# Performance work log

Measured on AMD Instinct MI355X. Metric: run time of the kernel, lower is better.

The kernel has to match this reference:

```python
import jax, jax.numpy as jnp
import numpy as np

D = 256      # dim
H = 8        # num_heads
HD = D // H  # head dim
P = 256      # patch_size
B = 4        # num clouds
L = 32768    # points per cloud (divisible by P)
N = B * L
MLP = int(D * 2.0)
PEH = max(32, D // 4)
EPS = 1e-5


def setup_inputs() -> dict:
    key = jax.random.key(0)
    ks = jax.random.split(key, 20)
    s = 0.02
    w = lambda k, shp: jax.random.normal(k, shp, jnp.float32) * s
    inp = {
        "feats": jax.random.normal(ks[0], (N, D), jnp.float32),
        "coord": jax.random.uniform(ks[1], (N, 3), jnp.float32),
        "lengths": jnp.full((B,), L, jnp.int32),
        # CoordPositionalEncoding: Linear(3,PEH) -> ReLU -> Linear(PEH,D)
        "pe_w1": w(ks[2], (3, PEH)), "pe_b1": jnp.zeros((PEH,), jnp.float32),
        "pe_w2": w(ks[3], (PEH, D)), "pe_b2": jnp.zeros((D,), jnp.float32),
        "pre_g": jnp.ones((D,), jnp.float32), "pre_b": jnp.zeros((D,), jnp.float32),
        # block: norm1 + MHA + norm2 + MLP
        "n1_g": jnp.ones((D,), jnp.float32), "n1_b": jnp.zeros((D,), jnp.float32),
        "wqkv": w(ks[4], (D, 3 * D)), "bqkv": jnp.zeros((3 * D,), jnp.float32),
        "wo": w(ks[5], (D, D)), "bo": jnp.zeros((D,), jnp.float32),
        "n2_g": jnp.ones((D,), jnp.float32), "n2_b": jnp.zeros((D,), jnp.float32),
        "m_w1": w(ks[6], (D, MLP)), "m_b1": jnp.zeros((MLP,), jnp.float32),
        "m_w2": w(ks[7], (MLP, D)), "m_b2": jnp.zeros((D,), jnp.float32),
        # global_gate: Linear(2D,D)->ReLU->Linear(D,D)->Sigmoid
        "gg_w1": w(ks[8], (2 * D, D)), "gg_b1": jnp.zeros((D,), jnp.float32),
        "gg_w2": w(ks[9], (D, D)), "gg_b2": jnp.zeros((D,), jnp.float32),
        # fuse: Linear(2D,D)->ReLU->Linear(D,D)
        "f_w1": w(ks[10], (2 * D, D)), "f_b1": jnp.zeros((D,), jnp.float32),
        "f_w2": w(ks[11], (D, D)), "f_b2": jnp.zeros((D,), jnp.float32),
    }
    return inp


def _ln(x, g, b):
    m = x.mean(-1, keepdims=True)
    v = jnp.mean((x - m) ** 2, -1, keepdims=True)
    return (x - m) * jax.lax.rsqrt(v + EPS) * g + b


def _sgca(feats, coord, lengths,
          pe_w1, pe_b1, pe_w2, pe_b2, pre_g, pre_b,
          n1_g, n1_b, wqkv, bqkv, wo, bo, n2_g, n2_b,
          m_w1, m_b1, m_w2, m_b2,
          gg_w1, gg_b1, gg_w2, gg_b2, f_w1, f_b1, f_w2, f_b2):
    Bn = lengths.shape[0]
    Ln = feats.shape[0] // Bn  # equal-length clouds

    def cloud(f, c):  # f: [L, D], c: [L, 3]
        # positional encoding (per-cloud centered / max-abs scaled coords)
        cc = c - c.mean(0, keepdims=True)
        scale = jnp.clip(jnp.abs(cc).max(0, keepdims=True), 1e-6)
        pe = jax.nn.relu((cc / scale) @ pe_w1 + pe_b1) @ pe_w2 + pe_b2
        x = _ln(f + pe, pre_g, pre_b)
        # serialization order from min-max normalized coords
        cn = c - c.min(0, keepdims=True)
        cn = cn / jnp.clip(cn.max(0, keepdims=True), 1e-6)
        key = cn[:, 0] + 2.17 * cn[:, 1] + 3.31 * cn[:, 2]
        order = jnp.argsort(key)
        xs = x[order].reshape(-1, P, D)  # [NP, P, D] block-diagonal windows
        # attention block (pre-norm MHA + residual)
        h = _ln(xs, n1_g, n1_b)
        qkv = h @ wqkv + bqkv
        q = qkv[..., :D].reshape(-1, P, H, HD)
        k = qkv[..., D:2 * D].reshape(-1, P, H, HD)
        v = qkv[..., 2 * D:].reshape(-1, P, H, HD)
        scores = jnp.einsum('nphd,nqhd->nhpq', q, k) / np.sqrt(HD).astype(np.float32)
        a = jax.nn.softmax(scores, axis=-1)
        o = jnp.einsum('nhpq,nqhd->nphd', a, v).reshape(-1, P, D)
        xs = xs + (o @ wo + bo)
        # MLP + residual
        xs = xs + (jax.nn.gelu(_ln(xs, n2_g, n2_b) @ m_w1 + m_b1, approximate=False) @ m_w2 + m_b2)
        # undo serialization
        xo = xs.reshape(-1, D)[jnp.argsort(order)]
        # global token gate/fuse
        gt = jnp.broadcast_to(xo.mean(0, keepdims=True), xo.shape)
        gate = jax.nn.sigmoid(jax.nn.relu(jnp.concatenate([f, gt], -1) @ gg_w1 + gg_b1) @ gg_w2 + gg_b2)
        fused = jax.nn.relu(jnp.concatenate([xo, gt], -1) @ f_w1 + f_b1) @ f_w2 + f_b2
        return f + gate * fused

    out = jax.vmap(cloud)(feats.reshape(Bn, Ln, D), coord.reshape(Bn, Ln, 3))
    return out.reshape(-1, D)


def reference(feats, coord, lengths,
              pe_w1, pe_b1, pe_w2, pe_b2, pre_g, pre_b,
              n1_g, n1_b, wqkv, bqkv, wo, bo, n2_g, n2_b,
              m_w1, m_b1, m_w2, m_b2,
              gg_w1, gg_b1, gg_w2, gg_b2, f_w1, f_b1, f_w2, f_b2):
    return _sgca(feats, coord, lengths,
                 pe_w1, pe_b1, pe_w2, pe_b2, pre_g, pre_b,
                 n1_g, n1_b, wqkv, bqkv, wo, bo, n2_g, n2_b,
                 m_w1, m_b1, m_w2, m_b2,
                 gg_w1, gg_b1, gg_w2, gg_b2, f_w1, f_b1, f_w2, f_b2)
```

## Files before the change

kernel.cpp:

```cpp
#include <hip/hip_runtime.h>
#include <hip/hip_bf16.h>
#include <math.h>

#define D_DIM 256
#define NHEAD 8
#define HDIM 32
#define PATCH 256
#define NCLOUD 4
#define LPC 32768
#define NTOT (NCLOUD * LPC)
#define MLPD 512
#define PEHID 64
#define LN_EPS 1e-5f
#define NCHUNK 4
#define CROWS (NTOT / NCHUNK)

typedef unsigned long long u64;
typedef unsigned short u16;
typedef short bf16x8 __attribute__((ext_vector_type(8)));
typedef float f32x4 __attribute__((ext_vector_type(4)));

__device__ __forceinline__ u16 f2bf(float x) {
  unsigned u = __float_as_uint(x);
  u += 0x7fffu + ((u >> 16) & 1u);
  return (u16)(u >> 16);
}
__device__ __forceinline__ float bf2f(u16 u) {
  return __uint_as_float(((unsigned)u) << 16);
}

__device__ __forceinline__ void gload_lds16(const u16* g, u16* l) {
  __builtin_amdgcn_global_load_lds((const __attribute__((address_space(1))) void*)g,
                                   (__attribute__((address_space(3))) void*)l, 16, 0, 0);
}

__global__ __launch_bounds__(256) void stats_kernel(const float* __restrict__ coord,
                                                    float* __restrict__ stats) {
  const int c = blockIdx.x, t = threadIdx.x;
  float sm[3] = {0.f, 0.f, 0.f};
  float mn[3] = {1e30f, 1e30f, 1e30f};
  float mx[3] = {-1e30f, -1e30f, -1e30f};
  const float* cp = coord + (size_t)c * LPC * 3;
  for (int i = t; i < LPC; i += 256) {
#pragma unroll
    for (int a = 0; a < 3; a++) {
      float v = cp[(size_t)i * 3 + a];
      sm[a] += v;
      mn[a] = fminf(mn[a], v);
      mx[a] = fmaxf(mx[a], v);
    }
  }
  __shared__ float sb[256];
  float rsum[3], rmn[3], rmx[3];
#pragma unroll
  for (int a = 0; a < 3; a++) {
    sb[t] = sm[a]; __syncthreads();
    for (int s = 128; s > 0; s >>= 1) { if (t < s) sb[t] += sb[t + s]; __syncthreads(); }
    rsum[a] = sb[0]; __syncthreads();
    sb[t] = mn[a]; __syncthreads();
    for (int s = 128; s > 0; s >>= 1) { if (t < s) sb[t] = fminf(sb[t], sb[t + s]); __syncthreads(); }
    rmn[a] = sb[0]; __syncthreads();
    sb[t] = mx[a]; __syncthreads();
    for (int s = 128; s > 0; s >>= 1) { if (t < s) sb[t] = fmaxf(sb[t], sb[t + s]); __syncthreads(); }
    rmx[a] = sb[0]; __syncthreads();
  }
  if (t == 0) {
    float* st = stats + c * 16;
#pragma unroll
    for (int a = 0; a < 3; a++) {
      float mean = rsum[a] / (float)LPC;
      st[a] = mean;
      st[3 + a] = fmaxf(fmaxf(rmx[a] - mean, mean - rmn[a]), 1e-6f);
      st[6 + a] = rmn[a];
      st[9 + a] = fmaxf(rmx[a] - rmn[a], 1e-6f);
    }
  }
}

__global__ __launch_bounds__(256) void key_kernel(const float* __restrict__ coord,
                                                  const float* __restrict__ stats,
                                                  u64* __restrict__ keys) {
#pragma clang fp contract(off)
  const int g = blockIdx.x * 256 + threadIdx.x;
  const int c = g >> 15;
  const float* st = stats + c * 16;
  float k0 = (coord[(size_t)g * 3 + 0] - st[6]) / st[9];
  float k1 = (coord[(size_t)g * 3 + 1] - st[7]) / st[10];
  float k2 = (coord[(size_t)g * 3 + 2] - st[8]) / st[11];
  float key = k0 + 2.17f * k1;
  key = key + 3.31f * k2;
  keys[g] = ((u64)__float_as_uint(key) << 32) | (unsigned)(g & (LPC - 1));
}

__global__ __launch_bounds__(1024) void sort_local_kernel(u64* __restrict__ keys) {
  __shared__ u64 s[4096];
  const int base = blockIdx.x * 4096;
  const int t = threadIdx.x;
  for (int i = t; i < 4096; i += 1024) s[i] = keys[base + i];
  __syncthreads();
  for (int k = 2; k <= 4096; k <<= 1) {
    for (int j = k >> 1; j > 0; j >>= 1) {
      for (int p = t; p < 2048; p += 1024) {
        int i = ((p & ~(j - 1)) << 1) | (p & (j - 1));
        int l = i | j;
        bool asc = (((base + i) & (LPC - 1)) & k) == 0;
        u64 a = s[i], bb = s[l];
        if (asc ? (a > bb) : (a < bb)) { s[i] = bb; s[l] = a; }
      }
      __syncthreads();
    }
  }
  for (int i = t; i < 4096; i += 1024) keys[base + i] = s[i];
}

__global__ __launch_bounds__(256) void sort_global_kernel(u64* __restrict__ keys, int k, int j) {
  int p = blockIdx.x * 256 + threadIdx.x;
  int i = ((p & ~(j - 1)) << 1) | (p & (j - 1));
  int l = i | j;
  bool asc = ((i & (LPC - 1)) & k) == 0;
  u64 a = keys[i], b = keys[l];
  if (asc ? (a > b) : (a < b)) { keys[i] = b; keys[l] = a; }
}

__global__ __launch_bounds__(1024) void sort_finish_kernel(u64* __restrict__ keys, int k) {
  __shared__ u64 s[4096];
  const int base = blockIdx.x * 4096;
  const int t = threadIdx.x;
  for (int i = t; i < 4096; i += 1024) s[i] = keys[base + i];
  __syncthreads();
  for (int j = 2048; j > 0; j >>= 1) {
    for (int p = t; p < 2048; p += 1024) {
      int i = ((p & ~(j - 1)) << 1) | (p & (j - 1));
      int l = i | j;
      bool asc = (((base + i) & (LPC - 1)) & k) == 0;
      u64 a = s[i], bb = s[l];
      if (asc ? (a > bb) : (a < bb)) { s[i] = bb; s[l] = a; }
    }
    __syncthreads();
  }
  for (int i = t; i < 4096; i += 1024) keys[base + i] = s[i];
}

__global__ __launch_bounds__(256) void rank_kernel(const u64* __restrict__ keys,
                                                   int* __restrict__ order,
                                                   int* __restrict__ rank) {
  const int g = blockIdx.x * 256 + threadIdx.x;
  const int src = (int)(unsigned)(keys[g] & 0xffffffffULL) + (g & ~(LPC - 1));
  order[g] = src;
  rank[src] = g;
}

__global__ __launch_bounds__(256) void wtrans_kernel(const float* __restrict__ src,
                                                     u16* __restrict__ dst, int R, int C) {
  __shared__ float t[32][33];
  const int bx = blockIdx.x * 32, by = blockIdx.y * 32;
  const int lc = threadIdx.x & 31, lr = threadIdx.x >> 5;
  for (int i = 0; i < 32; i += 8) t[lr + i][lc] = src[(size_t)(by + lr + i) * C + bx + lc];
  __syncthreads();
  for (int i = 0; i < 32; i += 8)
    dst[(size_t)(bx + lr + i) * R + by + lc] = f2bf(t[lc][lr + i]);
}

__global__ __launch_bounds__(256) void conv_bf16_kernel(const float* __restrict__ in,
                                                        u16* __restrict__ out) {
  size_t i = ((size_t)blockIdx.x * 256 + threadIdx.x) * 4;
  float4 v = *(const float4*)(in + i);
  ushort4 o;
  o.x = f2bf(v.x); o.y = f2bf(v.y); o.z = f2bf(v.z); o.w = f2bf(v.w);
  *(ushort4*)(out + i) = o;
}

__global__ __launch_bounds__(256) void h_kernel(const float* __restrict__ coord,
                                                const float* __restrict__ stats,
                                                const float* __restrict__ pw1,
                                                const float* __restrict__ pb1,
                                                u16* __restrict__ H) {
  const int idx = blockIdx.x * 256 + threadIdx.x;
  const int row = idx >> 6, j = idx & 63;
  const int c = row >> 15;
  const float* st = stats + c * 16;
  float s0 = (coord[(size_t)row * 3 + 0] - st[0]) / st[3];
  float s1 = (coord[(size_t)row * 3 + 1] - st[1]) / st[4];
  float s2 = (coord[(size_t)row * 3 + 2] - st[2]) / st[5];
  float h = pb1[j] + s0 * pw1[j] + s1 * pw1[64 + j] + s2 * pw1[128 + j];
  H[idx] = f2bf(fmaxf(h, 0.f));
}

__global__ __launch_bounds__(256) void add_ln_kernel(const float* __restrict__ feats,
                                                     const u16* __restrict__ pe,
                                                     const int* __restrict__ rank,
                                                     const float* __restrict__ g,
                                                     const float* __restrict__ b,
                                                     float* __restrict__ xs) {
  const int row = blockIdx.x * 4 + (threadIdx.x >> 6);
  const int lane = threadIdx.x & 63;
  float4 f = *(const float4*)(feats + (size_t)row * 256 + lane * 4);
  ushort4 p = *(const ushort4*)(pe + (size_t)row * 256 + lane * 4);
  float v0 = f.x + bf2f(p.x), v1 = f.y + bf2f(p.y);
  float v2 = f.z + bf2f(p.z), v3 = f.w + bf2f(p.w);
  float s = v0 + v1 + v2 + v3;
#pragma unroll
  for (int o = 32; o > 0; o >>= 1) s += __shfl_xor(s, o);
  float mean = s * (1.f / 256.f);
  float d0 = v0 - mean, d1 = v1 - mean, d2 = v2 - mean, d3 = v3 - mean;
  float ss = d0 * d0 + d1 * d1 + d2 * d2 + d3 * d3;
#pragma unroll
  for (int o = 32; o > 0; o >>= 1) ss += __shfl_xor(ss, o);
  float inv = 1.f / sqrtf(ss * (1.f / 256.f) + LN_EPS);
  float4 gv = *(const float4*)(g + lane * 4);
  float4 bv = *(const float4*)(b + lane * 4);
  int dst = rank[row];
  float4 o4;
  o4.x = d0 * inv * gv.x + bv.x; o4.y = d1 * inv * gv.y + bv.y;
  o4.z = d2 * inv * gv.z + bv.z; o4.w = d3 * inv * gv.w + bv.w;
  *(float4*)(xs + (size_t)dst * 256 + lane * 4) = o4;
}

__global__ __launch_bounds__(256) void ln_bf16_kernel(const float* __restrict__ in,
                                                      const float* __restrict__ g,
                                                      const float* __restrict__ b,
                                                      u16* __restrict__ out) {
  const int row = blockIdx.x * 4 + (threadIdx.x >> 6);
  const int lane = threadIdx.x & 63;
  float4 v = *(const float4*)(in + (size_t)row * 256 + lane * 4);
  float s = v.x + v.y + v.z + v.w;
#pragma unroll
  for (int o = 32; o > 0; o >>= 1) s += __shfl_xor(s, o);
  float mean = s * (1.f / 256.f);
  float d0 = v.x - mean, d1 = v.y - mean, d2 = v.z - mean, d3 = v.w - mean;
  float ss = d0 * d0 + d1 * d1 + d2 * d2 + d3 * d3;
#pragma unroll
  for (int o = 32; o > 0; o >>= 1) ss += __shfl_xor(ss, o);
  float inv = 1.f / sqrtf(ss * (1.f / 256.f) + LN_EPS);
  float4 gv = *(const float4*)(g + lane * 4);
  float4 bv = *(const float4*)(b + lane * 4);
  ushort4 o4;
  o4.x = f2bf(d0 * inv * gv.x + bv.x); o4.y = f2bf(d1 * inv * gv.y + bv.y);
  o4.z = f2bf(d2 * inv * gv.z + bv.z); o4.w = f2bf(d3 * inv * gv.w + bv.w);
  *(ushort4*)(out + (size_t)row * 256 + lane * 4) = o4;
}

template <int K, int ACT, int MODE, bool EXTRA>
__global__ __launch_bounds__(256, 4) void mfma_gemm(const u16* __restrict__ A,
                                                    const u16* __restrict__ Wt,
                                                    const float* __restrict__ bias,
                                                    const float* __restrict__ extra,
                                                    void* __restrict__ Cout, int Ko) {
  __shared__ __align__(16) u16 Al[128 * 32];
  __shared__ __align__(16) u16 Bl[128 * 32];
  const int tid = threadIdx.x;
  const int lane = tid & 63, wave = tid >> 6;
  const int wr = wave >> 1, wc = wave & 1;
  const int l15 = lane & 15, l4 = lane >> 4;
  const size_t row0 = (size_t)blockIdx.y * 128;
  const int col0 = blockIdx.x * 128;
  const int q0 = wave * 64 + lane;
  const int q1 = q0 + 256;
  const u16* gA0 = A + (row0 + (q0 >> 2)) * K + (q0 & 3) * 8;
  const u16* gA1 = A + (row0 + (q1 >> 2)) * K + (q1 & 3) * 8;
  const u16* gB0 = Wt + (size_t)(col0 + (q0 >> 2)) * K + (q0 & 3) * 8;
  const u16* gB1 = Wt + (size_t)(col0 + (q1 >> 2)) * K + (q1 & 3) * 8;
  u16* lA0 = Al + wave * 512;
  u16* lA1 = Al + 2048 + wave * 512;
  u16* lB0 = Bl + wave * 512;
  u16* lB1 = Bl + 2048 + wave * 512;
  f32x4 acc[4][4];
#pragma unroll
  for (int i = 0; i < 4; i++)
#pragma unroll
    for (int j = 0; j < 4; j++) acc[i][j] = f32x4{0.f, 0.f, 0.f, 0.f};
#pragma unroll 1
  for (int k0 = 0; k0 < K; k0 += 32) {
    gload_lds16(gA0 + k0, lA0);
    gload_lds16(gA1 + k0, lA1);
    gload_lds16(gB0 + k0, lB0);
    gload_lds16(gB1 + k0, lB1);
    __syncthreads();
    bf16x8 af[4], bfr[4];
#pragma unroll
    for (int rb = 0; rb < 4; rb++)
      af[rb] = *(const bf16x8*)&Al[(wr * 64 + rb * 16 + l15) * 32 + l4 * 8];
#pragma unroll
    for (int cb = 0; cb < 4; cb++)
      bfr[cb] = *(const bf16x8*)&Bl[(wc * 64 + cb * 16 + l15) * 32 + l4 * 8];
#pragma unroll
    for (int rb = 0; rb < 4; rb++)
#pragma unroll
      for (int cb = 0; cb < 4; cb++)
        acc[rb][cb] = __builtin_amdgcn_mfma_f32_16x16x32_bf16(af[rb], bfr[cb], acc[rb][cb], 0, 0, 0);
    __syncthreads();
  }
#pragma unroll
  for (int rb = 0; rb < 4; rb++)
#pragma unroll
    for (int cb = 0; cb < 4; cb++)
#pragma unroll
      for (int r = 0; r < 4; r++) {
        size_t row = row0 + wr * 64 + rb * 16 + l4 * 4 + r;
        int col = col0 + wc * 64 + cb * 16 + l15;
        float v = acc[rb][cb][r] + bias[col];
        if (EXTRA) v += extra[((int)(row >> 15)) * 256 + col];
        if (ACT == 1) v = fmaxf(v, 0.f);
        else if (ACT == 2) v = 0.5f * v * (1.f + erff(v * 0.70710678118654752440f));
        else if (ACT == 3) v = 1.f / (1.f + __expf(-v));
        size_t o = row * (size_t)Ko + col;
        if (MODE == 0) ((float*)Cout)[o] = v;
        else if (MODE == 1) ((float*)Cout)[o] += v;
        else ((u16*)Cout)[o] = f2bf(v);
      }
}

template <int K, int EPI>
__global__ __launch_bounds__(256, 3) void mfma_row_gemm(const u16* __restrict__ A,
                                                        const u16* __restrict__ Wt,
                                                        const float* __restrict__ bias,
                                                        float* __restrict__ xs,
                                                        u16* __restrict__ hout,
                                                        const int* __restrict__ order,
                                                        const float* __restrict__ g,
                                                        const float* __restrict__ b) {
  __shared__ __align__(16) u16 Al[64 * 32];
  __shared__ __align__(16) u16 Bl[256 * 32];
  __shared__ float reds[2][4][64];
  const int tid = threadIdx.x;
  const int lane = tid & 63, wave = tid >> 6;
  const int l15 = lane & 15, l4 = lane >> 4;
  const size_t row0 = (size_t)blockIdx.x * 64;
  const u16* gA = A + (row0 + (tid >> 2)) * K + (tid & 3) * 8;
  u16* lA = Al + wave * 512;
  const u16* gB[4];
  u16* lB[4];
#pragma unroll
  for (int s = 0; s < 4; s++) {
    int q = s * 256 + tid;
    gB[s] = Wt + (size_t)(q >> 2) * K + (q & 3) * 8;
    lB[s] = Bl + s * 2048 + wave * 512;
  }
  f32x4 acc[4][4];
#pragma unroll
  for (int i = 0; i < 4; i++)
#pragma unroll
    for (int j = 0; j < 4; j++) acc[i][j] = f32x4{0.f, 0.f, 0.f, 0.f};
#pragma unroll 1
  for (int k0 = 0; k0 < K; k0 += 32) {
    gload_lds16(gA + k0, lA);
#pragma unroll
    for (int s = 0; s < 4; s++) gload_lds16(gB[s] + k0, lB[s]);
    __syncthreads();
    bf16x8 af[4], bfr[4];
#pragma unroll
    for (int rb = 0; rb < 4; rb++)
      af[rb] = *(const bf16x8*)&Al[(rb * 16 + l15) * 32 + l4 * 8];
#pragma unroll
    for (int cb = 0; cb < 4; cb++)
      bfr[cb] = *(const bf16x8*)&Bl[(wave * 64 + cb * 16 + l15) * 32 + l4 * 8];
#pragma unroll
    for (int rb = 0; rb < 4; rb++)
#pragma unroll
      for (int cb = 0; cb < 4; cb++)
        acc[rb][cb] = __builtin_amdgcn_mfma_f32_16x16x32_bf16(af[rb], bfr[cb], acc[rb][cb], 0, 0, 0);
    __syncthreads();
  }
#pragma unroll
  for (int rb = 0; rb < 4; rb++)
#pragma unroll
    for (int cb = 0; cb < 4; cb++)
#pragma unroll
      for (int r = 0; r < 4; r++) {
        size_t row = row0 + rb * 16 + l4 * 4 + r;
        int col = wave * 64 + cb * 16 + l15;
        size_t o = row * 256 + col;
        float t = xs[o] + acc[rb][cb][r] + bias[col];
        xs[o] = t;
        acc[rb][cb][r] = t;
      }
  if (EPI == 1) {
    float ps[4][4];
#pragma unroll
    for (int rb = 0; rb < 4; rb++)
#pragma unroll
      for (int r = 0; r < 4; r++) {
        float v = acc[rb][0][r] + acc[rb][1][r] + acc[rb][2][r] + acc[rb][3][r];
#pragma unroll
        for (int oo = 1; oo < 16; oo <<= 1) v += __shfl_xor(v, oo);
        ps[rb][r] = v;
      }
    if (l15 == 0)
#pragma unroll
      for (int rb = 0; rb < 4; rb++)
#pragma unroll
        for (int r = 0; r < 4; r++) reds[0][wave][rb * 16 + l4 * 4 + r] = ps[rb][r];
    __syncthreads();
    float mean[4][4];
#pragma unroll
    for (int rb = 0; rb < 4; rb++)
#pragma unroll
      for (int r = 0; r < 4; r++) {
        int ri = rb * 16 + l4 * 4 + r;
        mean[rb][r] = (reds[0][0][ri] + reds[0][1][ri] + reds[0][2][ri] + reds[0][3][ri]) *
                      (1.f / 256.f);
      }
#pragma unroll
    for (int rb = 0; rb < 4; rb++)
#pragma unroll
      for (int r = 0; r < 4; r++) {
        float d0 = acc[rb][0][r] - mean[rb][r], d1 = acc[rb][1][r] - mean[rb][r];
        float d2 = acc[rb][2][r] - mean[rb][r], d3 = acc[rb][3][r] - mean[rb][r];
        float v = d0 * d0 + d1 * d1 + d2 * d2 + d3 * d3;
#pragma unroll
        for (int oo = 1; oo < 16; oo <<= 1) v += __shfl_xor(v, oo);
        ps[rb][r] = v;
      }
    if (l15 == 0)
#pragma unroll
      for (int rb = 0; rb < 4; rb++)
#pragma unroll
        for (int r = 0; r < 4; r++) reds[1][wave][rb * 16 + l4 * 4 + r] = ps[rb][r];
    __syncthreads();
#pragma unroll
    for (int rb = 0; rb < 4; rb++)
#pragma unroll
      for (int r = 0; r < 4; r++) {
        int ri = rb * 16 + l4 * 4 + r;
        float var = (reds[1][0][ri] + reds[1][1][ri] + reds[1][2][ri] + reds[1][3][ri]) *
                    (1.f / 256.f);
        float inv = 1.f / sqrtf(var + LN_EPS);
        size_t row = row0 + ri;
#pragma unroll
        for (int cb = 0; cb < 4; cb++) {
          int col = wave * 64 + cb * 16 + l15;
          hout[row * 256 + col] =
              f2bf((acc[rb][cb][r] - mean[rb][r]) * inv * g[col] + b[col]);
        }
      }
  } else {
#pragma unroll
    for (int rb = 0; rb < 4; rb++)
#pragma unroll
      for (int r = 0; r < 4; r++) {
        size_t row = row0 + rb * 16 + l4 * 4 + r;
        size_t dst = (size_t)order[row];
#pragma unroll
        for (int cb = 0; cb < 4; cb++) {
          int col = wave * 64 + cb * 16 + l15;
          hout[dst * 256 + col] = f2bf(acc[rb][cb][r]);
        }
      }
  }
}

__global__ __launch_bounds__(256, 3) void fuse2_kernel(const u16* __restrict__ A1,
                                                       const u16* __restrict__ A2,
                                                       const u16* __restrict__ B1t,
                                                       const u16* __restrict__ B2t,
                                                       const float* __restrict__ bias1,
                                                       const float* __restrict__ bias2,
                                                       const float* __restrict__ feats,
                                                       float* __restrict__ out) {
  __shared__ __align__(16) u16 A1l[128 * 32];
  __shared__ __align__(16) u16 A2l[128 * 32];
  __shared__ __align__(16) u16 B1l[64 * 32];
  __shared__ __align__(16) u16 B2l[64 * 32];
  const int tid = threadIdx.x;
  const int lane = tid & 63, wave = tid >> 6;
  const int l15 = lane & 15, l4 = lane >> 4;
  const size_t row0 = (size_t)blockIdx.y * 128;
  const int col0 = blockIdx.x * 64;
  const int q0 = tid, q1 = tid + 256;
  const size_t a0off = (row0 + (q0 >> 2)) * 256 + (q0 & 3) * 8;
  const size_t a1off = (row0 + (q1 >> 2)) * 256 + (q1 & 3) * 8;
  const size_t boff = (size_t)(col0 + (q0 >> 2)) * 256 + (q0 & 3) * 8;
  f32x4 acc1[2][4], acc2[2][4];
#pragma unroll
  for (int i = 0; i < 2; i++)
#pragma unroll
    for (int j = 0; j < 4; j++) {
      acc1[i][j] = f32x4{0.f, 0.f, 0.f, 0.f};
      acc2[i][j] = f32x4{0.f, 0.f, 0.f, 0.f};
    }
#pragma unroll 1
  for (int k0 = 0; k0 < 256; k0 += 32) {
    gload_lds16(A1 + a0off + k0, A1l + wave * 512);
    gload_lds16(A1 + a1off + k0, A1l + 2048 + wave * 512);
    gload_lds16(A2 + a0off + k0, A2l + wave * 512);
    gload_lds16(A2 + a1off + k0, A2l + 2048 + wave * 512);
    gload_lds16(B1t + boff + k0, B1l + wave * 512);
    gload_lds16(B2t + boff + k0, B2l + wave * 512);
    __syncthreads();
#pragma unroll
    for (int rb = 0; rb < 2; rb++) {
      bf16x8 a1f = *(const bf16x8*)&A1l[(wave * 32 + rb * 16 + l15) * 32 + l4 * 8];
      bf16x8 a2f = *(const bf16x8*)&A2l[(wave * 32 + rb * 16 + l15) * 32 + l4 * 8];
#pragma unroll
      for (int cb = 0; cb < 4; cb++) {
        bf16x8 b1f = *(const bf16x8*)&B1l[(cb * 16 + l15) * 32 + l4 * 8];
        bf16x8 b2f = *(const bf16x8*)&B2l[(cb * 16 + l15) * 32 + l4 * 8];
        acc1[rb][cb] = __builtin_amdgcn_mfma_f32_16x16x32_bf16(a1f, b1f, acc1[rb][cb], 0, 0, 0);
        acc2[rb][cb] = __builtin_amdgcn_mfma_f32_16x16x32_bf16(a2f, b2f, acc2[rb][cb], 0, 0, 0);
      }
    }
    __syncthreads();
  }
#pragma unroll
  for (int rb = 0; rb < 2; rb++)
#pragma unroll
    for (int cb = 0; cb < 4; cb++)
#pragma unroll
      for (int r = 0; r < 4; r++) {
        size_t row = row0 + wave * 32 + rb * 16 + l4 * 4 + r;
        int col = col0 + cb * 16 + l15;
        float gg = 1.f / (1.f + __expf(-(acc1[rb][cb][r] + bias1[col])));
        float fv = acc2[rb][cb][r] + bias2[col];
        size_t o = row * 256 + col;
        out[o] = feats[o] + gg * fv;
      }
}

__global__ __launch_bounds__(256, 3) void attn_mfma_kernel(const u16* __restrict__ qkv,
                                                           u16* __restrict__ ao) {
  __shared__ __align__(16) u16 VT[32 * 264];
  __shared__ __align__(16) u16 Pl[4][16 * 264];
  const int w = blockIdx.x, h = blockIdx.y;
  const int tid = threadIdx.x;
  const int lane = tid & 63, wave = tid >> 6;
  const int l15 = lane & 15, l4 = lane >> 4;
  const size_t base = (size_t)w * PATCH;
  {
    const u16* vrow = qkv + (base + tid) * 768 + 512 + h * HDIM;
#pragma unroll
    for (int d4 = 0; d4 < 8; d4++) {
      ushort4 v4 = *(const ushort4*)(vrow + d4 * 4);
      VT[(d4 * 4 + 0) * 264 + tid] = v4.x;
      VT[(d4 * 4 + 1) * 264 + tid] = v4.y;
      VT[(d4 * 4 + 2) * 264 + tid] = v4.z;
      VT[(d4 * 4 + 3) * 264 + tid] = v4.w;
    }
  }
  __syncthreads();
  u16* Pw = &Pl[wave][0];
  const float scale = 0.17677669529663687f;
  const f32x4 zero = {0.f, 0.f, 0.f, 0.f};
  for (int qt = 0; qt < 4; qt++) {
    const int qbase = wave * 64 + qt * 16;
    bf16x8 qf = *(const bf16x8*)(qkv + (base + qbase + l15) * 768 + h * HDIM + l4 * 8);
    f32x4 s[16];
#pragma unroll
    for (int kt = 0; kt < 16; kt++) {
      bf16x8 kf = *(const bf16x8*)(qkv + (base + kt * 16 + l15) * 768 + 256 + h * HDIM + l4 * 8);
      s[kt] = __builtin_amdgcn_mfma_f32_16x16x32_bf16(kf, qf, zero, 0, 0, 0);
    }
    float m = -1e30f;
#pragma unroll
    for (int kt = 0; kt < 16; kt++)
#pragma unroll
      for (int r = 0; r < 4; r++) { s[kt][r] *= scale; m = fmaxf(m, s[kt][r]); }
    m = fmaxf(m, __shfl_xor(m, 16));
    m = fmaxf(m, __shfl_xor(m, 32));
    float lsum = 0.f;
#pragma unroll
    for (int kt = 0; kt < 16; kt++) {
      float p0 = __expf(s[kt][0] - m), p1 = __expf(s[kt][1] - m);
      float p2 = __expf(s[kt][2] - m), p3 = __expf(s[kt][3] - m);
      lsum += (p0 + p1) + (p2 + p3);
      ushort4 pw4;
      pw4.x = f2bf(p0); pw4.y = f2bf(p1); pw4.z = f2bf(p2); pw4.w = f2bf(p3);
      *(ushort4*)&Pw[l15 * 264 + kt * 16 + l4 * 4] = pw4;
    }
    lsum += __shfl_xor(lsum, 16);
    lsum += __shfl_xor(lsum, 32);
    f32x4 o0 = zero, o1 = zero;
#pragma unroll
    for (int kc = 0; kc < 8; kc++) {
      bf16x8 pf = *(const bf16x8*)&Pw[l15 * 264 + kc * 32 + l4 * 8];
      bf16x8 va = *(const bf16x8*)&VT[l15 * 264 + kc * 32 + l4 * 8];
      bf16x8 vb = *(const bf16x8*)&VT[(16 + l15) * 264 + kc * 32 + l4 * 8];
      o0 = __builtin_amdgcn_mfma_f32_16x16x32_bf16(va, pf, o0, 0, 0, 0);
      o1 = __builtin_amdgcn_mfma_f32_16x16x32_bf16(vb, pf, o1, 0, 0, 0);
    }
    float inv = 1.f / lsum;
    u16* op = ao + (base + qbase + l15) * D_DIM + h * HDIM;
    ushort4 w0, w1;
    w0.x = f2bf(o0[0] * inv); w0.y = f2bf(o0[1] * inv);
    w0.z = f2bf(o0[2] * inv); w0.w = f2bf(o0[3] * inv);
    w1.x = f2bf(o1[0] * inv); w1.y = f2bf(o1[1] * inv);
    w1.z = f2bf(o1[2] * inv); w1.w = f2bf(o1[3] * inv);
    *(ushort4*)(op + l4 * 4) = w0;
    *(ushort4*)(op + 16 + l4 * 4) = w1;
  }
}

__global__ __launch_bounds__(256) void gt_partial_kernel(const float* __restrict__ xs,
                                                         float* __restrict__ part) {
  const int s = blockIdx.x, c = blockIdx.y;
  const int t = threadIdx.x;
  float acc = 0.f;
  const size_t base = (size_t)c * LPC + (size_t)s * 256;
  for (int r = 0; r < 256; r++) acc += xs[(base + r) * D_DIM + t];
  part[(size_t)(c * 128 + s) * D_DIM + t] = acc;
}

__global__ __launch_bounds__(256) void gt_reduce_kernel(const float* __restrict__ part,
                                                        float* __restrict__ gt) {
  const int c = blockIdx.x, t = threadIdx.x;
  float s = 0.f;
  for (int i = 0; i < 128; i++) s += part[(size_t)(c * 128 + i) * D_DIM + t];
  gt[c * D_DIM + t] = s * (1.f / (float)LPC);
}

__global__ __launch_bounds__(256) void pervec_kernel(const float* __restrict__ gt,
                                                     const float* __restrict__ ggw1,
                                                     const float* __restrict__ fw1,
                                                     float* __restrict__ ggt,
                                                     float* __restrict__ fgt) {
  const int c = blockIdx.x, which = blockIdx.y;
  const int t = threadIdx.x;
  const float* W = which ? fw1 : ggw1;
  float* o = which ? fgt : ggt;
  __shared__ float g[D_DIM];
  g[t] = gt[c * D_DIM + t];
  __syncthreads();
  float acc = 0.f;
#pragma unroll 8
  for (int k = 0; k < D_DIM; k++) acc += g[k] * W[(size_t)(256 + k) * D_DIM + t];
  o[c * D_DIM + t] = acc;
}

extern "C" void kernel_launch(void* const* d_in, const int* in_sizes, int n_in,
                              void* d_out, int out_size, void* d_ws, size_t ws_size,
                              hipStream_t stream) {
  const float* feats = (const float*)d_in[0];
  const float* coord = (const float*)d_in[1];
  const float* pe_w1 = (const float*)d_in[3];
  const float* pe_b1 = (const float*)d_in[4];
  const float* pe_w2 = (const float*)d_in[5];
  const float* pe_b2 = (const float*)d_in[6];
  const float* pre_g = (const float*)d_in[7];
  const float* pre_b = (const float*)d_in[8];
  const float* n1_g = (const float*)d_in[9];
  const float* n1_b = (const float*)d_in[10];
  const float* wqkv = (const float*)d_in[11];
  const float* bqkv = (const float*)d_in[12];
  const float* wo = (const float*)d_in[13];
  const float* bo = (const float*)d_in[14];
  const float* n2_g = (const float*)d_in[15];
  const float* n2_b = (const float*)d_in[16];
  const float* m_w1 = (const float*)d_in[17];
  const float* m_b1 = (const float*)d_in[18];
  const float* m_w2 = (const float*)d_in[19];
  const float* m_b2 = (const float*)d_in[20];
  const float* gg_w1 = (const float*)d_in[21];
  const float* gg_b1 = (const float*)d_in[22];
  const float* gg_w2 = (const float*)d_in[23];
  const float* gg_b2 = (const float*)d_in[24];
  const float* f_w1 = (const float*)d_in[25];
  const float* f_b1 = (const float*)d_in[26];
  const float* f_w2 = (const float*)d_in[27];
  const float* f_b2 = (const float*)d_in[28];
  float* out = (float*)d_out;

  char* ws = (char*)d_ws;
  float* xs = (float*)(ws);
  u16* hbuf = (u16*)(ws + 134217728);
  u16* qkvchunk = (u16*)(ws + 201326592);
  u16* aochunk = (u16*)(ws + 251658240);
  u16* tbuf = (u16*)(ws + 268435456);
  u16* Hbuf = (u16*)(ws + 268435456);
  u16* xobf = (u16*)(ws + 201326592);
  size_t off = 301989888;
  u64* keybuf = (u64*)(ws + off); off += (size_t)NTOT * 8;
  int* orderbuf = (int*)(ws + off); off += (size_t)NTOT * 4;
  int* rankbuf = (int*)(ws + off); off += (size_t)NTOT * 4;
  float* statsbuf = (float*)(ws + off); off += 4096;
  float* gtpart = (float*)(ws + off); off += (size_t)NCLOUD * 128 * D_DIM * 4;
  float* gtbuf = (float*)(ws + off); off += 4096;
  float* ggtbuf = (float*)(ws + off); off += 4096;
  float* fgtbuf = (float*)(ws + off); off += 4096;
  u16* wqkvT = (u16*)(ws + off); off += 768 * 256 * 2;
  u16* woT = (u16*)(ws + off); off += 256 * 256 * 2;
  u16* mw1T = (u16*)(ws + off); off += 512 * 256 * 2;
  u16* mw2T = (u16*)(ws + off); off += 256 * 512 * 2;
  u16* ggw1T = (u16*)(ws + off); off += 256 * 256 * 2;
  u16* ggw2T = (u16*)(ws + off); off += 256 * 256 * 2;
  u16* fw1T = (u16*)(ws + off); off += 256 * 256 * 2;
  u16* fw2T = (u16*)(ws + off); off += 256 * 256 * 2;
  u16* pw2T = (u16*)(ws + off); off += 64 * 256 * 2;
  u16* featsbf = (u16*)(ws);
  u16* u1buf = (u16*)(ws + 67108864);

  stats_kernel<<<NCLOUD, 256, 0, stream>>>(coord, statsbuf);
  key_kernel<<<NTOT / 256, 256, 0, stream>>>(coord, statsbuf, keybuf);
  sort_local_kernel<<<NTOT / 4096, 1024, 0, stream>>>(keybuf);
  for (int k = 8192; k <= 32768; k <<= 1) {
    for (int j = k >> 1; j >= 4096; j >>= 1)
      sort_global_kernel<<<NTOT / 512, 256, 0, stream>>>(keybuf, k, j);
    sort_finish_kernel<<<NTOT / 4096, 1024, 0, stream>>>(keybuf, k);
  }
  rank_kernel<<<NTOT / 256, 256, 0, stream>>>(keybuf, orderbuf, rankbuf);
  wtrans_kernel<<<dim3(24, 8), 256, 0, stream>>>(wqkv, wqkvT, 256, 768);
  wtrans_kernel<<<dim3(8, 8), 256, 0, stream>>>(wo, woT, 256, 256);
  wtrans_kernel<<<dim3(16, 8), 256, 0, stream>>>(m_w1, mw1T, 256, 512);
  wtrans_kernel<<<dim3(8, 16), 256, 0, stream>>>(m_w2, mw2T, 512, 256);
  wtrans_kernel<<<dim3(8, 8), 256, 0, stream>>>(gg_w1, ggw1T, 256, 256);
  wtrans_kernel<<<dim3(8, 8), 256, 0, stream>>>(gg_w2, ggw2T, 256, 256);
  wtrans_kernel<<<dim3(8, 8), 256, 0, stream>>>(f_w1, fw1T, 256, 256);
  wtrans_kernel<<<dim3(8, 8), 256, 0, stream>>>(f_w2, fw2T, 256, 256);
  wtrans_kernel<<<dim3(8, 2), 256, 0, stream>>>(pe_w2, pw2T, 64, 256);
  h_kernel<<<NTOT * 64 / 256, 256, 0, stream>>>(coord, statsbuf, pe_w1, pe_b1, Hbuf);
  mfma_gemm<64, 0, 2, false><<<dim3(2, NTOT / 128), 256, 0, stream>>>(
      Hbuf, pw2T, pe_b2, nullptr, hbuf, 256);
  add_ln_kernel<<<NTOT / 4, 256, 0, stream>>>(feats, hbuf, rankbuf, pre_g, pre_b, xs);
  ln_bf16_kernel<<<NTOT / 4, 256, 0, stream>>>(xs, n1_g, n1_b, hbuf);
  for (int ch = 0; ch < NCHUNK; ch++) {
    const size_t ro = (size_t)ch * CROWS;
    mfma_gemm<256, 0, 2, false><<<dim3(6, CROWS / 128), 256, 0, stream>>>(
        hbuf + ro * 256, wqkvT, bqkv, nullptr, qkvchunk, 768);
    attn_mfma_kernel<<<dim3(CROWS / PATCH, NHEAD), 256, 0, stream>>>(qkvchunk, aochunk);
    mfma_row_gemm<256, 1><<<CROWS / 64, 256, 0, stream>>>(
        aochunk, woT, bo, xs + ro * 256, hbuf + ro * 256, nullptr, n2_g, n2_b);
  }
  for (int ch = 0; ch < NCHUNK; ch++) {
    const size_t ro = (size_t)ch * CROWS;
    mfma_gemm<256, 2, 2, false><<<dim3(MLPD / 128, CROWS / 128), 256, 0, stream>>>(
        hbuf + ro * 256, mw1T, m_b1, nullptr, tbuf, 512);
    mfma_row_gemm<512, 2><<<CROWS / 64, 256, 0, stream>>>(
        tbuf, mw2T, m_b2, xs + ro * 256, xobf, orderbuf + ro, nullptr, nullptr);
  }
  gt_partial_kernel<<<dim3(128, NCLOUD), 256, 0, stream>>>(xs, gtpart);
  gt_reduce_kernel<<<NCLOUD, 256, 0, stream>>>(gtpart, gtbuf);
  pervec_kernel<<<dim3(NCLOUD, 2), 256, 0, stream>>>(gtbuf, gg_w1, f_w1, ggtbuf, fgtbuf);
  conv_bf16_kernel<<<NTOT * 256 / 1024, 256, 0, stream>>>(feats, featsbf);
  mfma_gemm<256, 1, 2, true><<<dim3(2, NTOT / 128), 256, 0, stream>>>(
      featsbf, ggw1T, gg_b1, ggtbuf, hbuf, 256);
  mfma_gemm<256, 1, 2, true><<<dim3(2, NTOT / 128), 256, 0, stream>>>(
      xobf, fw1T, f_b1, fgtbuf, u1buf, 256);
  fuse2_kernel<<<dim3(4, NTOT / 128), 256, 0, stream>>>(
      hbuf, u1buf, ggw2T, fw2T, gg_b2, f_b2, feats, out);
  (void)in_sizes; (void)n_in; (void)out_size; (void)ws_size;
}
```

Before: 1.398 ms.

## Fuse gate/fuse MLP tail into one kernel keeping intermediates in LDS

Replaces the bf16 conversion kernel, the two first-layer gate/fuse GEMMs and the second-layer fuse2 kernel with a single tail kernel. Each block processes 32 rows, converting feats to bf16 on the fly and keeping the ReLU hidden activations in shared memory, so the gate and fuse intermediates never round-trip through global memory. In exchange the row tile is small, so each block reloads the full 256x256 weight matrices four times per 32 rows. This raises weight traffic (mostly from L2) and lowers MFMA reuse per block compared with the previous 128-row tiles.

```diff
diff --git a/kernel.cpp b/kernel.cpp
--- a/kernel.cpp
+++ b/kernel.cpp
@@ -159,15 +159,6 @@
   __syncthreads();
   for (int i = 0; i < 32; i += 8)
     dst[(size_t)(bx + lr + i) * R + by + lc] = f2bf(t[lc][lr + i]);
-}
-
-__global__ __launch_bounds__(256) void conv_bf16_kernel(const float* __restrict__ in,
-                                                        u16* __restrict__ out) {
-  size_t i = ((size_t)blockIdx.x * 256 + threadIdx.x) * 4;
-  float4 v = *(const float4*)(in + i);
-  ushort4 o;
-  o.x = f2bf(v.x); o.y = f2bf(v.y); o.z = f2bf(v.z); o.w = f2bf(v.w);
-  *(ushort4*)(out + i) = o;
 }
 
 __global__ __launch_bounds__(256) void h_kernel(const float* __restrict__ coord,
@@ -449,55 +440,53 @@
   }
 }
 
-__global__ __launch_bounds__(256, 3) void fuse2_kernel(const u16* __restrict__ A1,
-                                                       const u16* __restrict__ A2,
-                                                       const u16* __restrict__ B1t,
-                                                       const u16* __restrict__ B2t,
-                                                       const float* __restrict__ bias1,
-                                                       const float* __restrict__ bias2,
-                                                       const float* __restrict__ feats,
-                                                       float* __restrict__ out) {
-  __shared__ __align__(16) u16 A1l[128 * 32];
-  __shared__ __align__(16) u16 A2l[128 * 32];
-  __shared__ __align__(16) u16 B1l[64 * 32];
-  __shared__ __align__(16) u16 B2l[64 * 32];
+__global__ __launch_bounds__(256, 3) void tail_kernel(
+    const float* __restrict__ feats, const u16* __restrict__ xobf,
+    const u16* __restrict__ ggw1T, const u16* __restrict__ fw1T,
+    const u16* __restrict__ ggw2T, const u16* __restrict__ fw2T,
+    const float* __restrict__ ggt, const float* __restrict__ fgt,
+    const float* __restrict__ b1g, const float* __restrict__ b1f,
+    const float* __restrict__ b2g, const float* __restrict__ b2f,
+    float* __restrict__ out) {
+  __shared__ __align__(16) u16 g1l[32 * 264];
+  __shared__ __align__(16) u16 u1l[32 * 264];
+  __shared__ __align__(16) u16 Bst[256 * 32];
+  __shared__ __align__(16) u16 Ast[32 * 32];
   const int tid = threadIdx.x;
   const int lane = tid & 63, wave = tid >> 6;
   const int l15 = lane & 15, l4 = lane >> 4;
-  const size_t row0 = (size_t)blockIdx.y * 128;
-  const int col0 = blockIdx.x * 64;
-  const int q0 = tid, q1 = tid + 256;
-  const size_t a0off = (row0 + (q0 >> 2)) * 256 + (q0 & 3) * 8;
-  const size_t a1off = (row0 + (q1 >> 2)) * 256 + (q1 & 3) * 8;
-  const size_t boff = (size_t)(col0 + (q0 >> 2)) * 256 + (q0 & 3) * 8;
-  f32x4 acc1[2][4], acc2[2][4];
+  const size_t row0 = (size_t)blockIdx.x * 32;
+  const int cloud = (int)(row0 >> 15);
+  f32x4 acc[2][4];
 #pragma unroll
   for (int i = 0; i < 2; i++)
 #pragma unroll
-    for (int j = 0; j < 4; j++) {
-      acc1[i][j] = f32x4{0.f, 0.f, 0.f, 0.f};
-      acc2[i][j] = f32x4{0.f, 0.f, 0.f, 0.f};
-    }
+    for (int j = 0; j < 4; j++) acc[i][j] = f32x4{0.f, 0.f, 0.f, 0.f};
 #pragma unroll 1
   for (int k0 = 0; k0 < 256; k0 += 32) {
-    gload_lds16(A1 + a0off + k0, A1l + wave * 512);
-    gload_lds16(A1 + a1off + k0, A1l + 2048 + wave * 512);
-    gload_lds16(A2 + a0off + k0, A2l + wave * 512);
-    gload_lds16(A2 + a1off + k0, A2l + 2048 + wave * 512);
-    gload_lds16(B1t + boff + k0, B1l + wave * 512);
-    gload_lds16(B2t + boff + k0, B2l + wave * 512);
-    __syncthreads();
-#pragma unroll
-    for (int rb = 0; rb < 2; rb++) {
-      bf16x8 a1f = *(const bf16x8*)&A1l[(wave * 32 + rb * 16 + l15) * 32 + l4 * 8];
-      bf16x8 a2f = *(const bf16x8*)&A2l[(wave * 32 + rb * 16 + l15) * 32 + l4 * 8];
-#pragma unroll
-      for (int cb = 0; cb < 4; cb++) {
-        bf16x8 b1f = *(const bf16x8*)&B1l[(cb * 16 + l15) * 32 + l4 * 8];
-        bf16x8 b2f = *(const bf16x8*)&B2l[(cb * 16 + l15) * 32 + l4 * 8];
-        acc1[rb][cb] = __builtin_amdgcn_mfma_f32_16x16x32_bf16(a1f, b1f, acc1[rb][cb], 0, 0, 0);
-        acc2[rb][cb] = __builtin_amdgcn_mfma_f32_16x16x32_bf16(a2f, b2f, acc2[rb][cb], 0, 0, 0);
-      }
+#pragma unroll
+    for (int s = 0; s < 4; s++) {
+      int q = s * 256 + tid;
+      gload_lds16(ggw1T + (size_t)(q >> 2) * 256 + k0 + (q & 3) * 8,
+                  Bst + s * 2048 + wave * 512);
+    }
+    {
+      int r = tid >> 3, c4 = (tid & 7) * 4;
+      float4 v = *(const float4*)(feats + (row0 + r) * 256 + k0 + c4);
+      ushort4 o4; o4.x = f2bf(v.x); o4.y = f2bf(v.y); o4.z = f2bf(v.z); o4.w = f2bf(v.w);
+      *(ushort4*)&Ast[r * 32 + c4] = o4;
+    }
+    __syncthreads();
+    bf16x8 af[2];
+#pragma unroll
+    for (int rb = 0; rb < 2; rb++)
+      af[rb] = *(const bf16x8*)&Ast[(rb * 16 + l15) * 32 + l4 * 8];
+#pragma unroll
+    for (int cb = 0; cb < 4; cb++) {
+      bf16x8 bf = *(const bf16x8*)&Bst[(wave * 64 + cb * 16 + l15) * 32 + l4 * 8];
+#pragma unroll
+      for (int rb = 0; rb < 2; rb++)
+        acc[rb][cb] = __builtin_amdgcn_mfma_f32_16x16x32_bf16(af[rb], bf, acc[rb][cb], 0, 0, 0);
     }
     __syncthreads();
   }
@@ -507,12 +496,124 @@
     for (int cb = 0; cb < 4; cb++)
 #pragma unroll
       for (int r = 0; r < 4; r++) {
-        size_t row = row0 + wave * 32 + rb * 16 + l4 * 4 + r;
-        int col = col0 + cb * 16 + l15;
-        float gg = 1.f / (1.f + __expf(-(acc1[rb][cb][r] + bias1[col])));
-        float fv = acc2[rb][cb][r] + bias2[col];
+        int row = rb * 16 + l4 * 4 + r;
+        int col = wave * 64 + cb * 16 + l15;
+        float v = acc[rb][cb][r] + b1g[col] + ggt[cloud * 256 + col];
+        g1l[row * 264 + col] = f2bf(fmaxf(v, 0.f));
+      }
+#pragma unroll
+  for (int i = 0; i < 2; i++)
+#pragma unroll
+    for (int j = 0; j < 4; j++) acc[i][j] = f32x4{0.f, 0.f, 0.f, 0.f};
+#pragma unroll 1
+  for (int k0 = 0; k0 < 256; k0 += 32) {
+    __syncthreads();
+#pragma unroll
+    for (int s = 0; s < 4; s++) {
+      int q = s * 256 + tid;
+      gload_lds16(fw1T + (size_t)(q >> 2) * 256 + k0 + (q & 3) * 8,
+                  Bst + s * 2048 + wave * 512);
+    }
+    if (tid < 128) {
+      int q = tid;
+      gload_lds16(xobf + (row0 + (q >> 2)) * 256 + k0 + (q & 3) * 8, Ast + wave * 512);
+    }
+    __syncthreads();
+    bf16x8 af[2];
+#pragma unroll
+    for (int rb = 0; rb < 2; rb++)
+      af[rb] = *(const bf16x8*)&Ast[(rb * 16 + l15) * 32 + l4 * 8];
+#pragma unroll
+    for (int cb = 0; cb < 4; cb++) {
+      bf16x8 bf = *(const bf16x8*)&Bst[(wave * 64 + cb * 16 + l15) * 32 + l4 * 8];
+#pragma unroll
+      for (int rb = 0; rb < 2; rb++)
+        acc[rb][cb] = __builtin_amdgcn_mfma_f32_16x16x32_bf16(af[rb], bf, acc[rb][cb], 0, 0, 0);
+    }
+  }
+#pragma unroll
+  for (int rb = 0; rb < 2; rb++)
+#pragma unroll
+    for (int cb = 0; cb < 4; cb++)
+#pragma unroll
+      for (int r = 0; r < 4; r++) {
+        int row = rb * 16 + l4 * 4 + r;
+        int col = wave * 64 + cb * 16 + l15;
+        float v = acc[rb][cb][r] + b1f[col] + fgt[cloud * 256 + col];
+        u1l[row * 264 + col] = f2bf(fmaxf(v, 0.f));
+      }
+#pragma unroll
+  for (int i = 0; i < 2; i++)
+#pragma unroll
+    for (int j = 0; j < 4; j++) acc[i][j] = f32x4{0.f, 0.f, 0.f, 0.f};
+#pragma unroll 1
+  for (int k0 = 0; k0 < 256; k0 += 32) {
+    __syncthreads();
+#pragma unroll
+    for (int s = 0; s < 4; s++) {
+      int q = s * 256 + tid;
+      gload_lds16(ggw2T + (size_t)(q >> 2) * 256 + k0 + (q & 3) * 8,
+                  Bst + s * 2048 + wave * 512);
+    }
+    __syncthreads();
+    bf16x8 af[2];
+#pragma unroll
+    for (int rb = 0; rb < 2; rb++)
+      af[rb] = *(const bf16x8*)&g1l[(rb * 16 + l15) * 264 + k0 + l4 * 8];
+#pragma unroll
+    for (int cb = 0; cb < 4; cb++) {
+      bf16x8 bf = *(const bf16x8*)&Bst[(wave * 64 + cb * 16 + l15) * 32 + l4 * 8];
+#pragma unroll
+      for (int rb = 0; rb < 2; rb++)
+        acc[rb][cb] = __builtin_amdgcn_mfma_f32_16x16x32_bf16(af[rb], bf, acc[rb][cb], 0, 0, 0);
+    }
+  }
+  float sg[2][4][4];
+#pragma unroll
+  for (int rb = 0; rb < 2; rb++)
+#pragma unroll
+    for (int cb = 0; cb < 4; cb++)
+#pragma unroll
+      for (int r = 0; r < 4; r++) {
+        int col = wave * 64 + cb * 16 + l15;
+        sg[rb][cb][r] = 1.f / (1.f + __expf(-(acc[rb][cb][r] + b2g[col])));
+      }
+#pragma unroll
+  for (int i = 0; i < 2; i++)
+#pragma unroll
+    for (int j = 0; j < 4; j++) acc[i][j] = f32x4{0.f, 0.f, 0.f, 0.f};
+#pragma unroll 1
+  for (int k0 = 0; k0 < 256; k0 += 32) {
+    __syncthreads();
+#pragma unroll
+    for (int s = 0; s < 4; s++) {
+      int q = s * 256 + tid;
+      gload_lds16(fw2T + (size_t)(q >> 2) * 256 + k0 + (q & 3) * 8,
+                  Bst + s * 2048 + wave * 512);
+    }
+    __syncthreads();
+    bf16x8 af[2];
+#pragma unroll
+    for (int rb = 0; rb < 2; rb++)
+      af[rb] = *(const bf16x8*)&u1l[(rb * 16 + l15) * 264 + k0 + l4 * 8];
+#pragma unroll
+    for (int cb = 0; cb < 4; cb++) {
+      bf16x8 bf = *(const bf16x8*)&Bst[(wave * 64 + cb * 16 + l15) * 32 + l4 * 8];
+#pragma unroll
+      for (int rb = 0; rb < 2; rb++)
+        acc[rb][cb] = __builtin_amdgcn_mfma_f32_16x16x32_bf16(af[rb], bf, acc[rb][cb], 0, 0, 0);
+    }
+  }
+#pragma unroll
+  for (int rb = 0; rb < 2; rb++)
+#pragma unroll
+    for (int cb = 0; cb < 4; cb++)
+#pragma unroll
+      for (int r = 0; r < 4; r++) {
+        size_t row = row0 + rb * 16 + l4 * 4 + r;
+        int col = wave * 64 + cb * 16 + l15;
         size_t o = row * 256 + col;
-        out[o] = feats[o] + gg * fv;
+        out[o] = feats[o] + sg[rb][cb][r] * (acc[rb][cb][r] + b2f[col]);
       }
 }
 
@@ -684,8 +785,6 @@
   u16* fw1T = (u16*)(ws + off); off += 256 * 256 * 2;
   u16* fw2T = (u16*)(ws + off); off += 256 * 256 * 2;
   u16* pw2T = (u16*)(ws + off); off += 64 * 256 * 2;
-  u16* featsbf = (u16*)(ws);
-  u16* u1buf = (u16*)(ws + 67108864);
 
   stats_kernel<<<NCLOUD, 256, 0, stream>>>(coord, statsbuf);
   key_kernel<<<NTOT / 256, 256, 0, stream>>>(coord, statsbuf, keybuf);
@@ -728,12 +827,7 @@
   gt_partial_kernel<<<dim3(128, NCLOUD), 256, 0, stream>>>(xs, gtpart);
   gt_reduce_kernel<<<NCLOUD, 256, 0, stream>>>(gtpart, gtbuf);
   pervec_kernel<<<dim3(NCLOUD, 2), 256, 0, stream>>>(gtbuf, gg_w1, f_w1, ggtbuf, fgtbuf);
-  conv_bf16_kernel<<<NTOT * 256 / 1024, 256, 0, stream>>>(feats, featsbf);
-  mfma_gemm<256, 1, 2, true><<<dim3(2, NTOT / 128), 256, 0, stream>>>(
-      featsbf, ggw1T, gg_b1, ggtbuf, hbuf, 256);
-  mfma_gemm<256, 1, 2, true><<<dim3(2, NTOT / 128), 256, 0, stream>>>(
-      xobf, fw1T, f_b1, fgtbuf, u1buf, 256);
-  fuse2_kernel<<<dim3(4, NTOT / 128), 256, 0, stream>>>(
-      hbuf, u1buf, ggw2T, fw2T, gg_b2, f_b2, feats, out);
+  tail_kernel<<<NTOT / 32, 256, 0, stream>>>(feats, xobf, ggw1T, fw1T, ggw2T, fw2T,
+                                             ggtbuf, fgtbuf, gg_b1, f_b1, gg_b2, f_b2, out);
   (void)in_sizes; (void)n_in; (void)out_size; (void)ws_size;
 }
```

Measured after the change: 1.359 ms. 1.03x faster.
